# Kernel tuning notes

Hardware: AMD Instinct MI355X
Metric: run time of the kernel (lower is better)

The kernel has to match this reference:

```python
import jax, jax.numpy as jnp
import numpy as np

C = 384          # input_channels
DH = 768         # dim_hidden
WS = 7           # window size (kernel_size)
NH = 12          # num_heads
HID = 3072       # mlp hidden = dim_hidden * mlp_ratio
NP = WS * WS     # 49 patch tokens
N = NP + 1       # + 1 cls token
SCALE = (C // NH) ** -0.5
REL_DIM = 2 * WS - 1


def _rel_pos_index():
    r = np.arange(WS)
    qx, qy = np.meshgrid(r, r, indexing='ij')
    q = np.stack([qx.ravel(), qy.ravel()], -1)                 # [NP,2], row-major flatten
    rel = q[:, None, :] - q[None, :, :] + WS - 1               # [NP,NP,2], values in [0,2ws-2]
    return jnp.asarray(rel[..., 0] * REL_DIM + rel[..., 1])    # [NP,NP]

REL_IDX = _rel_pos_index()


def layer_norm(x, g, b, eps=1e-5):
    m = jnp.mean(x, axis=-1, keepdims=True)
    v = jnp.var(x, axis=-1, keepdims=True)
    return (x - m) * jax.lax.rsqrt(v + eps) * g + b


def attention(x, w_qkv, w_proj, b_proj, rel_pos=None, mask=None):
    Bx, Nx, Cx = x.shape
    qkv = (x @ w_qkv.T).reshape(Bx, Nx, 3, NH, Cx // NH).transpose(2, 0, 3, 1, 4)
    q, k, v = qkv[0], qkv[1], qkv[2]                           # [B,H,N,d]
    attn = jnp.einsum('bhqd,bhkd->bhqk', q, k) * SCALE
    if rel_pos is not None:
        bias = rel_pos[REL_IDX].transpose(2, 0, 1)[None]       # [1,NH,NP,NP]
        attn = attn.at[:, :, 1:, 1:].add(bias)                 # skip cls token row/col
    if mask is not None:
        attn = attn + mask[:, None]                            # broadcast over heads
    attn = jax.nn.softmax(attn, axis=-1)
    y = jnp.einsum('bhqk,bhkd->bhqd', attn, v).transpose(0, 2, 1, 3).reshape(Bx, Nx, Cx)
    return y @ w_proj.T + b_proj


def setup_inputs() -> dict:
    key = jax.random.key(0)
    ks = jax.random.split(key, 16)
    s = 0.02
    BNW = 2048  # B * num_windows = 32 * 64
    return {
        'out': jax.random.normal(ks[0], (BNW, N, C), jnp.float32),
        'mask': jnp.zeros((BNW, N, N), jnp.float32),
        'g0': jnp.ones((C,), jnp.float32), 'b0': jnp.zeros((C,), jnp.float32),
        'g1': jnp.ones((C,), jnp.float32), 'b1': jnp.zeros((C,), jnp.float32),
        'g2': jnp.ones((C,), jnp.float32), 'b2': jnp.zeros((C,), jnp.float32),
        'ge': jnp.ones((C,), jnp.float32), 'be': jnp.zeros((C,), jnp.float32),
        'w_qkv': jax.random.normal(ks[1], (3 * C, C), jnp.float32) * s,
        'w_proj': jax.random.normal(ks[2], (C, C), jnp.float32) * s,
        'b_proj': jnp.zeros((C,), jnp.float32),
        'rel_pos': jax.random.normal(ks[3], (REL_DIM * REL_DIM, NH), jnp.float32) * s,
        'w_fc1': jax.random.normal(ks[4], (HID, C), jnp.float32) * s,
        'b_fc1': jnp.zeros((HID,), jnp.float32),
        'w_fc2': jax.random.normal(ks[5], (DH, HID), jnp.float32) * s,
        'b_fc2': jnp.zeros((DH,), jnp.float32),
        'w_exp': jax.random.normal(ks[6], (DH, C), jnp.float32) * s,
        'b_exp': jnp.zeros((DH,), jnp.float32),
        'w_lin': jax.random.normal(ks[7], (C, DH), jnp.float32) * s,
        'b_lin': jnp.zeros((C,), jnp.float32),
        'B': 32, 'H': 56, 'W': 56,
    }


def reference(out, mask, g0, b0, g1, b1, g2, b2, ge, be,
              w_qkv, w_proj, b_proj, rel_pos,
              w_fc1, b_fc1, w_fc2, b_fc2, w_exp, b_exp, w_lin, b_lin,
              B, H, W):
    Cc = out.shape[-1]
    # cls-token attention across windows of each image
    cls = out[:, :1].reshape(B, -1, Cc)                        # [B, nw, C]
    cls = cls + attention(layer_norm(cls, g0, b0), w_qkv, w_proj, b_proj)
    cls = cls.reshape(-1, 1, Cc)
    x = jnp.concatenate([cls, out[:, 1:]], axis=1)             # [B*nw, N, C]
    # windowed patch attention with rel-pos bias + mask
    x = x + attention(layer_norm(x, g1, b1), w_qkv, w_proj, b_proj,
                      rel_pos=rel_pos, mask=mask)
    # expand path: norm -> gelu -> linear (input_channels != dim_hidden)
    identity = jax.nn.gelu(layer_norm(x, ge, be), approximate=False) @ w_exp.T + b_exp
    # mlp path: norm -> fc1 -> gelu -> fc2
    h = layer_norm(x, g2, b2)
    h = jax.nn.gelu(h @ w_fc1.T + b_fc1, approximate=False)
    h = h @ w_fc2.T + b_fc2
    tmp = identity + h                                          # [B*nw, N, DH]
    return tmp @ w_lin.T + b_lin                                # [B*nw, N, C]
```

## Files before the change

### kernel.cpp

```cpp
#include <hip/hip_runtime.h>
#include <hip/hip_bf16.h>
#include <math.h>

#define NHEADS 12
#define NTOK   50
#define NWIN   2048
#define IMGS   32
#define CDIM   384
#define QKVD   1152
#define DHID   768
#define MLPH   3072
#define KTAIL  3456
#define SCALE_F 0.17677669529663687f

typedef short short8 __attribute__((ext_vector_type(8)));
typedef short short4v __attribute__((ext_vector_type(4)));
typedef short short2v __attribute__((ext_vector_type(2)));
typedef float f32x4  __attribute__((ext_vector_type(4)));
typedef __hip_bfloat16 bf16;

__device__ __forceinline__ float rcp_fast(float x){ return __builtin_amdgcn_rcpf(x); }

__device__ __forceinline__ float gelu_f(float x){
  float z = 0.7978845608028654f*(x + 0.044715f*x*x*x);
  float e = __expf(2.0f*z);
  return 0.5f*x*(1.0f + (1.0f - 2.0f*rcp_fast(e+1.0f)));
}
__device__ __forceinline__ float gelu_fast(float x){
  float e = __expf(-1.702f*x);
  return x * rcp_fast(1.0f + e);
}
__device__ __forceinline__ short bfs(float x){
  bf16 h = __float2bfloat16(x); return *(short*)&h;
}

__global__ void cvt4_kernel(const float* s0, bf16* d0, int n0,
                            const float* s1, bf16* d1, int n1,
                            const float* s2, bf16* d2, int n2,
                            const float* s3, bf16* d3, int n3){
  int stride = gridDim.x*blockDim.x, g = blockIdx.x*blockDim.x + threadIdx.x;
  for (int i=g; i<n0; i+=stride) d0[i] = __float2bfloat16(s0[i]);
  for (int i=g; i<n1; i+=stride) d1[i] = __float2bfloat16(s1[i]);
  for (int i=g; i<n2; i+=stride) d2[i] = __float2bfloat16(s2[i]);
  for (int i=g; i<n3; i+=stride) d3[i] = __float2bfloat16(s3[i]);
}

__global__ __launch_bounds__(256) void transpose_cvt_kernel(const float* __restrict__ src,
    bf16* __restrict__ dst, int R, int Cc){
  __shared__ float tile[32][33];
  int bx = blockIdx.x, by = blockIdx.y;
  int c = threadIdx.x & 31, r0 = threadIdx.x >> 5;
  #pragma unroll
  for (int rr = r0; rr < 32; rr += 8)
    tile[rr][c] = src[(size_t)(by*32+rr)*Cc + bx*32 + c];
  __syncthreads();
  #pragma unroll
  for (int rr = r0; rr < 32; rr += 8)
    dst[(size_t)(bx*32+rr)*R + by*32 + c] = __float2bfloat16(tile[c][rr]);
}

__global__ void bias_combine_kernel(const float* __restrict__ wlin,
    const float* __restrict__ b_lin, const float* __restrict__ b_exp,
    const float* __restrict__ b_fc2, float* __restrict__ biasc){
  int i = blockIdx.x*blockDim.x + threadIdx.x;
  if (i >= CDIM) return;
  float s = b_lin[i];
  for (int d=0; d<DHID; d++) s += wlin[(size_t)i*DHID+d]*(b_exp[d]+b_fc2[d]);
  biasc[i] = s;
}

template<bool GELU>
__global__ __launch_bounds__(256) void ln_kernel(const float* __restrict__ x, long ldx,
    const float* __restrict__ g, const float* __restrict__ b,
    bf16* __restrict__ y, int rows)
{
  int row = blockIdx.x*4 + (threadIdx.x>>6);
  if (row >= rows) return;
  int l = threadIdx.x & 63;
  const float2* xr = (const float2*)(x + (size_t)row*ldx);
  float2 v[3]; float s = 0.f;
  #pragma unroll
  for (int j=0;j<3;j++){ v[j] = xr[l + 64*j]; s += v[j].x + v[j].y; }
  #pragma unroll
  for (int off=32; off; off>>=1) s += __shfl_xor(s, off, 64);
  float mean = s * (1.0f/384.0f);
  float vs = 0.f;
  #pragma unroll
  for (int j=0;j<3;j++){ float dx=v[j].x-mean, dy=v[j].y-mean; vs += dx*dx+dy*dy; }
  #pragma unroll
  for (int off=32; off; off>>=1) vs += __shfl_xor(vs, off, 64);
  float rstd = rsqrtf(vs*(1.0f/384.0f) + 1e-5f);
  short2v* yr = (short2v*)(y + (size_t)row*384);
  const float2* gv = (const float2*)g; const float2* bv = (const float2*)b;
  #pragma unroll
  for (int j=0;j<3;j++){
    float2 gg = gv[l+64*j], bb = bv[l+64*j];
    float o0 = (v[j].x-mean)*rstd*gg.x + bb.x;
    float o1 = (v[j].y-mean)*rstd*gg.y + bb.y;
    if (GELU){ o0 = gelu_f(o0); o1 = gelu_f(o1); }
    short2v pk; pk[0]=bfs(o0); pk[1]=bfs(o1);
    yr[l+64*j] = pk;
  }
}

__global__ __launch_bounds__(256) void ln_sel_kernel(const float* __restrict__ xa,
    const float* __restrict__ xbse,
    const float* __restrict__ g, const float* __restrict__ b,
    bf16* __restrict__ y, int rows)
{
  int row = blockIdx.x*4 + (threadIdx.x>>6);
  if (row >= rows) return;
  int l = threadIdx.x & 63;
  const float* src = (row % 50 == 0) ? xa : xbse;
  const float2* xr = (const float2*)(src + (size_t)row*384);
  float2 v[3]; float s = 0.f;
  #pragma unroll
  for (int j=0;j<3;j++){ v[j] = xr[l + 64*j]; s += v[j].x + v[j].y; }
  #pragma unroll
  for (int off=32; off; off>>=1) s += __shfl_xor(s, off, 64);
  float mean = s * (1.0f/384.0f);
  float vs = 0.f;
  #pragma unroll
  for (int j=0;j<3;j++){ float dx=v[j].x-mean, dy=v[j].y-mean; vs += dx*dx+dy*dy; }
  #pragma unroll
  for (int off=32; off; off>>=1) vs += __shfl_xor(vs, off, 64);
  float rstd = rsqrtf(vs*(1.0f/384.0f) + 1e-5f);
  short2v* yr = (short2v*)(y + (size_t)row*384);
  const float2* gv = (const float2*)g; const float2* bv = (const float2*)b;
  #pragma unroll
  for (int j=0;j<3;j++){
    float2 gg = gv[l+64*j], bb = bv[l+64*j];
    short2v pk;
    pk[0]=bfs((v[j].x-mean)*rstd*gg.x + bb.x);
    pk[1]=bfs((v[j].y-mean)*rstd*gg.y + bb.y);
    yr[l+64*j] = pk;
  }
}

__global__ __launch_bounds__(256) void ln_dual_kernel(const float* __restrict__ x,
    const float* __restrict__ ge, const float* __restrict__ be,
    const float* __restrict__ g2, const float* __restrict__ b2,
    bf16* __restrict__ yeo, long lde, bf16* __restrict__ y2o, int rows)
{
  int row = blockIdx.x*4 + (threadIdx.x>>6);
  if (row >= rows) return;
  int l = threadIdx.x & 63;
  const float2* xr = (const float2*)(x + (size_t)row*384);
  float2 v[3]; float s = 0.f;
  #pragma unroll
  for (int j=0;j<3;j++){ v[j] = xr[l + 64*j]; s += v[j].x + v[j].y; }
  #pragma unroll
  for (int off=32; off; off>>=1) s += __shfl_xor(s, off, 64);
  float mean = s * (1.0f/384.0f);
  float vs = 0.f;
  #pragma unroll
  for (int j=0;j<3;j++){ float dx=v[j].x-mean, dy=v[j].y-mean; vs += dx*dx+dy*dy; }
  #pragma unroll
  for (int off=32; off; off>>=1) vs += __shfl_xor(vs, off, 64);
  float rstd = rsqrtf(vs*(1.0f/384.0f) + 1e-5f);
  short2v* ye = (short2v*)(yeo + (size_t)row*lde);
  short2v* y2 = (short2v*)(y2o + (size_t)row*384);
  const float2* gev = (const float2*)ge; const float2* bev = (const float2*)be;
  const float2* g2v = (const float2*)g2; const float2* b2v = (const float2*)b2;
  #pragma unroll
  for (int j=0;j<3;j++){
    float n0 = (v[j].x-mean)*rstd, n1 = (v[j].y-mean)*rstd;
    float2 gg = gev[l+64*j], bb = bev[l+64*j];
    short2v pe; pe[0]=bfs(gelu_f(n0*gg.x+bb.x)); pe[1]=bfs(gelu_f(n1*gg.y+bb.y));
    ye[l+64*j] = pe;
    gg = g2v[l+64*j]; bb = b2v[l+64*j];
    short2v p2; p2[0]=bfs(n0*gg.x+bb.x); p2[1]=bfs(n1*gg.y+bb.y);
    y2[l+64*j] = p2;
  }
}

template<bool OUT_BF16, bool BIAS, int RES, int GELU>
__device__ __forceinline__ void gemm_dev(
    const bf16* __restrict__ A, const bf16* __restrict__ B, void* Cv,
    const float* __restrict__ bias, const void* res, const void* res2,
    int M, int N, int K, int lda, int ldb, int ldc, int ldres)
{
  __shared__ short As[3][128*32];
  __shared__ short Bs[3][128*32];
  const int t  = threadIdx.x;
  const int l  = t & 63;
  const int w  = t >> 6;
  const int wr = w >> 1, wc = w & 1;
  const int lr = l & 15, kg = l >> 4;

  const int nwg = gridDim.x * gridDim.y;
  const int lin = blockIdx.y * gridDim.x + blockIdx.x;
  const int q8 = nwg >> 3, r8 = nwg & 7;
  const int xcd = lin & 7, slot = lin >> 3;
  const int swz = (xcd < r8) ? (xcd*(q8+1) + slot) : (r8*(q8+1) + (xcd-r8)*q8 + slot);
  const int by = swz / gridDim.x, bx = swz - by*gridDim.x;

  const int bm = by * 128, bn = bx * 128;
  const short* Ag = (const short*)A;
  const short* Bg = (const short*)B;

  const int eo0 = w*1024 + l*8;
  const int rowS0 = eo0 >> 5, colS0 = eo0 & 31;
  const int eo1 = eo0 + 512;
  const int rowS1 = eo1 >> 5, colS1 = eo1 & 31;

  #define STAGE(k0, b) do { \
    __builtin_amdgcn_global_load_lds( \
      (const __attribute__((address_space(1))) void*)&Ag[(size_t)(bm+rowS0)*lda + (k0) + colS0], \
      (__attribute__((address_space(3))) void*)((char*)&As[b][0] + w*2048), 16, 0, 0); \
    __builtin_amdgcn_global_load_lds( \
      (const __attribute__((address_space(1))) void*)&Bg[(size_t)(bn+rowS0)*ldb + (k0) + colS0], \
      (__attribute__((address_space(3))) void*)((char*)&Bs[b][0] + w*2048), 16, 0, 0); \
    __builtin_amdgcn_global_load_lds( \
      (const __attribute__((address_space(1))) void*)&Ag[(size_t)(bm+rowS1)*lda + (k0) + colS1], \
      (__attribute__((address_space(3))) void*)((char*)&As[b][0] + w*2048 + 1024), 16, 0, 0); \
    __builtin_amdgcn_global_load_lds( \
      (const __attribute__((address_space(1))) void*)&Bg[(size_t)(bn+rowS1)*ldb + (k0) + colS1], \
      (__attribute__((address_space(3))) void*)((char*)&Bs[b][0] + w*2048 + 1024), 16, 0, 0); \
  } while(0)

  f32x4 acc[4][4] = {};

  STAGE(0, 0);
  STAGE(32, 1);
  asm volatile("s_waitcnt vmcnt(4)" ::: "memory");
  __builtin_amdgcn_s_barrier();

  int cur = 0, nb = 2;
  for (int k0 = 0; k0 < K; k0 += 32) {
    const bool more = (k0 + 64 < K);
    if (more) STAGE(k0 + 64, nb);

    short8 af[4], bfm[4];
    #pragma unroll
    for (int m=0;m<4;m++) af[m]  = *(const short8*)(&As[cur][(wr*64 + m*16 + lr)*32 + kg*8]);
    #pragma unroll
    for (int n=0;n<4;n++) bfm[n] = *(const short8*)(&Bs[cur][(wc*64 + n*16 + lr)*32 + kg*8]);
    __builtin_amdgcn_s_setprio(1);
    #pragma unroll
    for (int m=0;m<4;m++)
      #pragma unroll
      for (int n=0;n<4;n++)
        acc[m][n] = __builtin_amdgcn_mfma_f32_16x16x32_bf16(af[m], bfm[n], acc[m][n], 0,0,0);
    __builtin_amdgcn_s_setprio(0);

    if (more) { asm volatile("s_waitcnt vmcnt(4)" ::: "memory"); }
    else      { asm volatile("s_waitcnt vmcnt(0)" ::: "memory"); }
    __builtin_amdgcn_s_barrier();
    cur = (cur==2) ? 0 : cur+1;
    nb  = (nb==2)  ? 0 : nb+1;
  }
  #undef STAGE

  #pragma unroll
  for (int m=0;m<4;m++){
    int row0 = bm + wr*64 + m*16 + kg*4;
    #pragma unroll
    for (int n=0;n<4;n++){
      int col = bn + wc*64 + n*16 + lr;
      float bv = BIAS ? bias[col] : 0.0f;
      #pragma unroll
      for (int r=0;r<4;r++){
        float val = acc[m][n][r] + bv;
        if (RES == 1) val += ((const float*)res)[(size_t)(row0+r)*ldres + col];
        if (RES == 3){
          int grow = row0 + r;
          const float* rs = ((grow % 50) == 0) ? (const float*)res : (const float*)res2;
          val += rs[(size_t)grow*ldres + col];
        }
        if (GELU == 1) val = gelu_fast(val);
        if (OUT_BF16) ((bf16*)Cv)[(size_t)(row0+r)*ldc + col] = __float2bfloat16(val);
        else          ((float*)Cv)[(size_t)(row0+r)*ldc + col] = val;
      }
    }
  }
}

#define GEMM_K(NAME, OB, BI, RE, GE) \
__global__ __launch_bounds__(256) void NAME( \
    const bf16* __restrict__ A, const bf16* __restrict__ B, void* Cv, \
    const float* __restrict__ bias, const void* res, const void* res2, \
    int M, int N, int K, int lda, int ldc, int ldres){ \
  gemm_dev<OB,BI,RE,GE>(A,B,Cv,bias,res,res2,M,N,K,lda,K,ldc,ldres); }

GEMM_K(gemm_qkv_k,   true,  false, 0, 0)
GEMM_K(gemm_projc_k, false, true,  1, 0)
GEMM_K(gemm_projw_k, false, true,  3, 0)
GEMM_K(gemm_fc1_k,   true,  true,  0, 1)
GEMM_K(gemm_tail_k,  false, true,  0, 0)
GEMM_K(gemm_wcmb_k,  true,  false, 0, 0)

__global__ __launch_bounds__(256) void attn_cls_kernel(const bf16* __restrict__ qkv,
                                                       bf16* __restrict__ y)
{
  int img = blockIdx.x, h = blockIdx.y;
  __shared__ float q[64][33], k[64][33], v[64][33];
  __shared__ float s[64][65];
  int t = threadIdx.x;
  for (int idx=t; idx<64*32; idx+=256){
    int i = idx>>5, d = idx&31;
    const bf16* base = qkv + ((size_t)(img*64+i))*QKVD + h*32 + d;
    q[i][d] = __bfloat162float(base[0]);
    k[i][d] = __bfloat162float(base[384]);
    v[i][d] = __bfloat162float(base[768]);
  }
  __syncthreads();
  for (int idx=t; idx<64*64; idx+=256){
    int i = idx>>6, j = idx&63;
    float a = 0.f;
    #pragma unroll
    for (int d=0; d<32; d++) a += q[i][d]*k[j][d];
    s[i][j] = a * SCALE_F;
  }
  __syncthreads();
  if (t < 64){
    float m = -1e30f;
    for (int j=0;j<64;j++) m = fmaxf(m, s[t][j]);
    float sum = 0.f;
    for (int j=0;j<64;j++){ float e = __expf(s[t][j]-m); s[t][j]=e; sum+=e; }
    float inv = rcp_fast(sum);
    for (int j=0;j<64;j++) s[t][j] *= inv;
  }
  __syncthreads();
  for (int idx=t; idx<64*32; idx+=256){
    int i = idx>>5, d = idx&31;
    float a = 0.f;
    for (int j=0;j<64;j++) a += s[i][j]*v[j][d];
    y[((size_t)(img*64+i))*CDIM + h*32 + d] = __float2bfloat16(a);
  }
}

__global__ __launch_bounds__(64) void attn_win_mfma(const bf16* __restrict__ qkv,
    const float* __restrict__ mask, const float* __restrict__ rel_pos,
    bf16* __restrict__ y)
{
  const int lw = blockIdx.x, h = blockIdx.y;
  const int l = threadIdx.x;
  const int lr = l & 15, kg = l >> 4;
  __shared__ short Plds[64*72];
  __shared__ short VTl[32*72];
  __shared__ float rp[169];

  const size_t tok0 = (size_t)lw * NTOK;
  const short* qbase = (const short*)qkv;

  for (int i=l; i<169; i+=64) rp[i] = rel_pos[i*NHEADS + h];

  short8 qf[4], kf[4];
  #pragma unroll
  for (int n=0;n<4;n++){
    int qt = 16*n + lr;
    if (qt < 50) qf[n] = *(const short8*)&qbase[(tok0+qt)*QKVD + h*32 + kg*8];
    else         qf[n] = short8(0);
  }
  #pragma unroll
  for (int m=0;m<4;m++){
    int kt = 16*m + lr;
    if (kt < 50) kf[m] = *(const short8*)&qbase[(tok0+kt)*QKVD + 384 + h*32 + kg*8];
    else         kf[m] = short8(0);
  }

  {
    short vv[32];
    if (l < 50){
      const short8* vp = (const short8*)&qbase[(tok0+l)*QKVD + 768 + h*32];
      #pragma unroll
      for (int jj=0;jj<4;jj++){ short8 xv = vp[jj];
        #pragma unroll
        for (int e=0;e<8;e++) vv[jj*8+e] = xv[e]; }
    } else {
      #pragma unroll
      for (int d=0; d<32; d++) vv[d]=0;
    }
    #pragma unroll
    for (int d=0; d<32; d++) VTl[d*72 + l] = vv[d];
  }

  f32x4 sacc[4][4] = {};
  #pragma unroll
  for (int m=0;m<4;m++)
    #pragma unroll
    for (int n=0;n<4;n++)
      sacc[m][n] = __builtin_amdgcn_mfma_f32_16x16x32_bf16(kf[m], qf[n], sacc[m][n], 0,0,0);

  const float* mrow = mask + (size_t)lw*2500;
  float sv[4][4][4];
  #pragma unroll
  for (int m=0;m<4;m++){
    #pragma unroll
    for (int r=0;r<4;r++){
      int kt = 16*m + 4*kg + r;
      #pragma unroll
      for (int n=0;n<4;n++){
        int qt = 16*n + lr;
        float a;
        if (kt < 50 && qt < 50){
          a = sacc[m][n][r] * SCALE_F;
          if (kt>=1 && qt>=1){
            int qi=qt-1, kj=kt-1;
            int ridx = ((qi/7)-(kj/7)+6)*13 + (qi%7)-(kj%7)+6;
            a += rp[ridx];
          }
          a += mrow[qt*50+kt];
        } else a = -1e30f;
        sv[m][r][n] = a;
      }
    }
  }

  #pragma unroll
  for (int n=0;n<4;n++){
    float mx = -1e30f;
    #pragma unroll
    for (int m=0;m<4;m++)
      #pragma unroll
      for (int r=0;r<4;r++) mx = fmaxf(mx, sv[m][r][n]);
    mx = fmaxf(mx, __shfl_xor(mx, 16));
    mx = fmaxf(mx, __shfl_xor(mx, 32));
    float sum = 0.f;
    float pv[4][4];
    #pragma unroll
    for (int m=0;m<4;m++)
      #pragma unroll
      for (int r=0;r<4;r++){ float p = __expf(sv[m][r][n]-mx); pv[m][r]=p; sum+=p; }
    sum += __shfl_xor(sum, 16);
    sum += __shfl_xor(sum, 32);
    float inv = rcp_fast(sum);
    int qrow = (16*n + lr)*72;
    #pragma unroll
    for (int m=0;m<4;m++){
      short4v pk;
      #pragma unroll
      for (int r=0;r<4;r++) pk[r] = bfs(pv[m][r]*inv);
      *(short4v*)&Plds[qrow + 16*m + 4*kg] = pk;
    }
  }
  __syncthreads();

  f32x4 oacc[2][4] = {};
  #pragma unroll
  for (int ks=0; ks<2; ks++){
    short8 pf[4];
    #pragma unroll
    for (int n=0;n<4;n++)
      pf[n] = *(const short8*)&Plds[(16*n+lr)*72 + 32*ks + kg*8];
    #pragma unroll
    for (int md=0; md<2; md++){
      short8 vf = *(const short8*)&VTl[(16*md+lr)*72 + 32*ks + kg*8];
      #pragma unroll
      for (int n=0;n<4;n++)
        oacc[md][n] = __builtin_amdgcn_mfma_f32_16x16x32_bf16(vf, pf[n], oacc[md][n], 0,0,0);
    }
  }

  short* yb = (short*)y;
  #pragma unroll
  for (int n=0;n<4;n++){
    int qt = 16*n + lr;
    if (qt >= 50) continue;
    #pragma unroll
    for (int md=0; md<2; md++){
      short4v pk;
      #pragma unroll
      for (int r=0;r<4;r++) pk[r] = bfs(oacc[md][n][r]);
      *(short4v*)&yb[(tok0+qt)*CDIM + h*32 + 16*md + 4*kg] = pk;
    }
  }
}

extern "C" void kernel_launch(void* const* d_in, const int* in_sizes, int n_in,
                              void* d_out, int out_size, void* d_ws, size_t ws_size,
                              hipStream_t stream)
{
  const float* x_in   = (const float*)d_in[0];
  const float* maskp  = (const float*)d_in[1];
  const float* g0 = (const float*)d_in[2];  const float* b0 = (const float*)d_in[3];
  const float* g1 = (const float*)d_in[4];  const float* b1 = (const float*)d_in[5];
  const float* g2 = (const float*)d_in[6];  const float* b2 = (const float*)d_in[7];
  const float* ge = (const float*)d_in[8];  const float* be = (const float*)d_in[9];
  const float* w_qkv = (const float*)d_in[10];
  const float* w_proj= (const float*)d_in[11];
  const float* b_proj= (const float*)d_in[12];
  const float* rel_pos=(const float*)d_in[13];
  const float* w_fc1 = (const float*)d_in[14];
  const float* b_fc1 = (const float*)d_in[15];
  const float* w_fc2 = (const float*)d_in[16];
  const float* b_fc2 = (const float*)d_in[17];
  const float* w_exp = (const float*)d_in[18];
  const float* b_exp = (const float*)d_in[19];
  const float* w_lin = (const float*)d_in[20];
  const float* b_lin = (const float*)d_in[21];
  float* dout = (float*)d_out;

  const size_t NT = (size_t)NWIN * NTOK;

  size_t off = 0;
  auto alloc = [&](size_t bytes)->void* {
    void* p = (char*)d_ws + off;
    off += (bytes + 255) & ~(size_t)255;
    return p;
  };

  bf16* wqkv_b = (bf16*)alloc((size_t)QKVD*CDIM*2);
  bf16* wproj_b= (bf16*)alloc((size_t)CDIM*CDIM*2);
  bf16* wfc1_b = (bf16*)alloc((size_t)MLPH*CDIM*2);
  bf16* wlin_b = (bf16*)alloc((size_t)CDIM*DHID*2);
  bf16* wexpT_b= (bf16*)alloc((size_t)CDIM*DHID*2);
  bf16* wfc2T_b= (bf16*)alloc((size_t)MLPH*DHID*2);
  bf16* W_comb = (bf16*)alloc((size_t)CDIM*KTAIL*2);
  float* biasc = (float*)alloc((size_t)CDIM*4);
  float* xb    = (float*)alloc(NT*CDIM*4);
  bf16* clsln  = (bf16*)alloc((size_t)NWIN*CDIM*2);
  bf16* qkvcls = (bf16*)alloc((size_t)NWIN*QKVD*2);
  bf16* ycls   = (bf16*)alloc((size_t)NWIN*CDIM*2);

  int CH_W = 2048;
  const size_t per_window = 422400ull;
  while (CH_W > 128 && off + (size_t)CH_W*per_window + 16384 > ws_size) CH_W >>= 1;
  const int CH_T = CH_W * NTOK;

  bf16*  xln   = (bf16*) alloc((size_t)CH_T*CDIM*2);
  bf16*  ybfc  = (bf16*) alloc((size_t)CH_T*CDIM*2);
  bf16*  h1ext = (bf16*) alloc((size_t)CH_T*KTAIL*2);
  bf16*  qkvc  = h1ext;

  cvt4_kernel<<<512, 256, 0, stream>>>(
      w_qkv, wqkv_b, QKVD*CDIM,  w_proj, wproj_b, CDIM*CDIM,
      w_fc1, wfc1_b, MLPH*CDIM,  w_lin,  wlin_b,  CDIM*DHID);
  transpose_cvt_kernel<<<dim3(CDIM/32, DHID/32), 256, 0, stream>>>(w_exp, wexpT_b, DHID, CDIM);
  transpose_cvt_kernel<<<dim3(MLPH/32, DHID/32), 256, 0, stream>>>(w_fc2, wfc2T_b, DHID, MLPH);
  bias_combine_kernel<<<6, 64, 0, stream>>>(w_lin, b_lin, b_exp, b_fc2, biasc);
  gemm_wcmb_k<<<dim3(CDIM/128, CDIM/128), 256, 0, stream>>>(
      wlin_b, wexpT_b, W_comb, nullptr, nullptr, nullptr, CDIM, CDIM, DHID, DHID, KTAIL, 0);
  gemm_wcmb_k<<<dim3(MLPH/128, CDIM/128), 256, 0, stream>>>(
      wlin_b, wfc2T_b, W_comb + 384, nullptr, nullptr, nullptr, CDIM, MLPH, DHID, DHID, KTAIL, 0);

  ln_kernel<false><<<NWIN/4, 256, 0, stream>>>(x_in, (long)NTOK*CDIM, g0, b0, clsln, NWIN);
  gemm_qkv_k<<<dim3(QKVD/128, NWIN/128), 256, 0, stream>>>(
      clsln, wqkv_b, qkvcls, nullptr, nullptr, nullptr, NWIN, QKVD, CDIM, CDIM, QKVD, 0);
  attn_cls_kernel<<<dim3(IMGS, NHEADS), 256, 0, stream>>>(qkvcls, ycls);
  gemm_projc_k<<<dim3(CDIM/128, NWIN/128), 256, 0, stream>>>(
      ycls, wproj_b, xb, b_proj, x_in, nullptr, NWIN, CDIM, CDIM, CDIM, NTOK*CDIM, NTOK*CDIM);

  const int nch = NWIN / CH_W;
  for (int c = 0; c < nch; c++){
    int w0 = c * CH_W;
    size_t t0 = (size_t)w0 * NTOK;
    float* xbc = xb + t0*CDIM;
    const float* xinc = x_in + t0*CDIM;
    float* doutc = dout + t0*CDIM;
    int MT = CH_T, MB = CH_T/128;

    ln_sel_kernel<<<MT/4, 256, 0, stream>>>(xbc, xinc, g1, b1, xln, MT);
    gemm_qkv_k<<<dim3(QKVD/128, MB), 256, 0, stream>>>(
        xln, wqkv_b, qkvc, nullptr, nullptr, nullptr, MT, QKVD, CDIM, CDIM, QKVD, 0);
    attn_win_mfma<<<dim3(CH_W, NHEADS), 64, 0, stream>>>(
        qkvc, maskp + (size_t)w0*2500, rel_pos, ybfc);
    gemm_projw_k<<<dim3(CDIM/128, MB), 256, 0, stream>>>(
        ybfc, wproj_b, xbc, b_proj, xbc, xinc, MT, CDIM, CDIM, CDIM, CDIM, CDIM);

    ln_dual_kernel<<<MT/4, 256, 0, stream>>>(xbc, ge, be, g2, b2, h1ext, KTAIL, ybfc, MT);

    gemm_fc1_k<<<dim3(MLPH/128, MB), 256, 0, stream>>>(
        ybfc, wfc1_b, h1ext + 384, b_fc1, nullptr, nullptr, MT, MLPH, CDIM, CDIM, KTAIL, 0);

    gemm_tail_k<<<dim3(CDIM/128, MB), 256, 0, stream>>>(
        h1ext, W_comb, doutc, biasc, nullptr, nullptr, MT, CDIM, KTAIL, KTAIL, CDIM, 0);
  }
}
```

Baseline: 1.654 ms.

## Process all heads per window block and stage mask in shared memory

The windowed attention kernel now launches one 128-thread block per window instead of one 64-thread block per (window, head). The block loads the 50x50 mask into LDS once, and each of its two wavefronts loops over six heads, so the mask is reused across all twelve heads instead of being re-read from global memory per head. The tail GEMM is also specialised with a compile-time ldb constant. In exchange the grid has twelve times fewer blocks, each with more LDS and serial work, which may reduce parallelism and latency hiding.

```diff
diff --git a/kernel.cpp b/kernel.cpp
--- a/kernel.cpp
+++ b/kernel.cpp
@@ -287,8 +287,14 @@
 GEMM_K(gemm_projc_k, false, true,  1, 0)
 GEMM_K(gemm_projw_k, false, true,  3, 0)
 GEMM_K(gemm_fc1_k,   true,  true,  0, 1)
-GEMM_K(gemm_tail_k,  false, true,  0, 0)
 GEMM_K(gemm_wcmb_k,  true,  false, 0, 0)
+
+__global__ __launch_bounds__(256) void gemm_tail_k(
+    const bf16* __restrict__ A, const bf16* __restrict__ B, void* Cv,
+    const float* __restrict__ bias, const void* res, const void* res2,
+    int M, int N, int K, int lda, int ldc, int ldres){
+  gemm_dev<false,true,0,0>(A,B,Cv,bias,res,res2,M,N,K,lda,KTAIL,ldc,ldres);
+}
 
 __global__ __launch_bounds__(256) void attn_cls_kernel(const bf16* __restrict__ qkv,
                                                        bf16* __restrict__ y)
@@ -330,140 +336,153 @@
   }
 }
 
-__global__ __launch_bounds__(64) void attn_win_mfma(const bf16* __restrict__ qkv,
+__global__ __launch_bounds__(128) void attn_win_mfma(const bf16* __restrict__ qkv,
     const float* __restrict__ mask, const float* __restrict__ rel_pos,
     bf16* __restrict__ y)
 {
-  const int lw = blockIdx.x, h = blockIdx.y;
-  const int l = threadIdx.x;
+  const int lw = blockIdx.x;
+  const int tid = threadIdx.x;
+  const int w = tid >> 6;
+  const int l = tid & 63;
   const int lr = l & 15, kg = l >> 4;
-  __shared__ short Plds[64*72];
-  __shared__ short VTl[32*72];
-  __shared__ float rp[169];
+
+  __shared__ float msk[2500];
+  __shared__ float rp_w[2][169];
+  __shared__ short PldsA[2][64*72];
+  __shared__ short VTlA[2][32*72];
 
   const size_t tok0 = (size_t)lw * NTOK;
   const short* qbase = (const short*)qkv;
 
-  for (int i=l; i<169; i+=64) rp[i] = rel_pos[i*NHEADS + h];
-
-  short8 qf[4], kf[4];
-  #pragma unroll
-  for (int n=0;n<4;n++){
-    int qt = 16*n + lr;
-    if (qt < 50) qf[n] = *(const short8*)&qbase[(tok0+qt)*QKVD + h*32 + kg*8];
-    else         qf[n] = short8(0);
-  }
-  #pragma unroll
-  for (int m=0;m<4;m++){
-    int kt = 16*m + lr;
-    if (kt < 50) kf[m] = *(const short8*)&qbase[(tok0+kt)*QKVD + 384 + h*32 + kg*8];
-    else         kf[m] = short8(0);
-  }
-
-  {
-    short vv[32];
-    if (l < 50){
-      const short8* vp = (const short8*)&qbase[(tok0+l)*QKVD + 768 + h*32];
-      #pragma unroll
-      for (int jj=0;jj<4;jj++){ short8 xv = vp[jj];
-        #pragma unroll
-        for (int e=0;e<8;e++) vv[jj*8+e] = xv[e]; }
-    } else {
-      #pragma unroll
-      for (int d=0; d<32; d++) vv[d]=0;
-    }
-    #pragma unroll
-    for (int d=0; d<32; d++) VTl[d*72 + l] = vv[d];
-  }
-
-  f32x4 sacc[4][4] = {};
-  #pragma unroll
-  for (int m=0;m<4;m++)
-    #pragma unroll
-    for (int n=0;n<4;n++)
-      sacc[m][n] = __builtin_amdgcn_mfma_f32_16x16x32_bf16(kf[m], qf[n], sacc[m][n], 0,0,0);
-
-  const float* mrow = mask + (size_t)lw*2500;
-  float sv[4][4][4];
-  #pragma unroll
-  for (int m=0;m<4;m++){
-    #pragma unroll
-    for (int r=0;r<4;r++){
-      int kt = 16*m + 4*kg + r;
-      #pragma unroll
-      for (int n=0;n<4;n++){
-        int qt = 16*n + lr;
-        float a;
-        if (kt < 50 && qt < 50){
-          a = sacc[m][n][r] * SCALE_F;
-          if (kt>=1 && qt>=1){
-            int qi=qt-1, kj=kt-1;
-            int ridx = ((qi/7)-(kj/7)+6)*13 + (qi%7)-(kj%7)+6;
-            a += rp[ridx];
-          }
-          a += mrow[qt*50+kt];
-        } else a = -1e30f;
-        sv[m][r][n] = a;
+  for (int i = tid; i < 2500; i += 128) msk[i] = mask[(size_t)lw*2500 + i];
+  __syncthreads();
+
+  short* Plds = &PldsA[w][0];
+  short* VTl  = &VTlA[w][0];
+  float* rp   = &rp_w[w][0];
+
+  for (int hh = 0; hh < 6; hh++){
+    const int h = w*6 + hh;
+
+    for (int i = l; i < 169; i += 64) rp[i] = rel_pos[i*NHEADS + h];
+
+    short8 qf[4], kf[4];
+    #pragma unroll
+    for (int n=0;n<4;n++){
+      int qt = 16*n + lr;
+      if (qt < 50) qf[n] = *(const short8*)&qbase[(tok0+qt)*QKVD + h*32 + kg*8];
+      else         qf[n] = short8(0);
+    }
+    #pragma unroll
+    for (int m=0;m<4;m++){
+      int kt = 16*m + lr;
+      if (kt < 50) kf[m] = *(const short8*)&qbase[(tok0+kt)*QKVD + 384 + h*32 + kg*8];
+      else         kf[m] = short8(0);
+    }
+
+    {
+      short vv[32];
+      if (l < 50){
+        const short8* vp = (const short8*)&qbase[(tok0+l)*QKVD + 768 + h*32];
+        #pragma unroll
+        for (int jj=0;jj<4;jj++){ short8 xv = vp[jj];
+          #pragma unroll
+          for (int e=0;e<8;e++) vv[jj*8+e] = xv[e]; }
+      } else {
+        #pragma unroll
+        for (int d=0; d<32; d++) vv[d]=0;
       }
-    }
-  }
-
-  #pragma unroll
-  for (int n=0;n<4;n++){
-    float mx = -1e30f;
+      #pragma unroll
+      for (int d=0; d<32; d++) VTl[d*72 + l] = vv[d];
+    }
+
+    f32x4 sacc[4][4] = {};
     #pragma unroll
     for (int m=0;m<4;m++)
       #pragma unroll
-      for (int r=0;r<4;r++) mx = fmaxf(mx, sv[m][r][n]);
-    mx = fmaxf(mx, __shfl_xor(mx, 16));
-    mx = fmaxf(mx, __shfl_xor(mx, 32));
-    float sum = 0.f;
-    float pv[4][4];
-    #pragma unroll
-    for (int m=0;m<4;m++)
-      #pragma unroll
-      for (int r=0;r<4;r++){ float p = __expf(sv[m][r][n]-mx); pv[m][r]=p; sum+=p; }
-    sum += __shfl_xor(sum, 16);
-    sum += __shfl_xor(sum, 32);
-    float inv = rcp_fast(sum);
-    int qrow = (16*n + lr)*72;
+      for (int n=0;n<4;n++)
+        sacc[m][n] = __builtin_amdgcn_mfma_f32_16x16x32_bf16(kf[m], qf[n], sacc[m][n], 0,0,0);
+
+    float sv[4][4][4];
     #pragma unroll
     for (int m=0;m<4;m++){
-      short4v pk;
-      #pragma unroll
-      for (int r=0;r<4;r++) pk[r] = bfs(pv[m][r]*inv);
-      *(short4v*)&Plds[qrow + 16*m + 4*kg] = pk;
-    }
-  }
-  __syncthreads();
-
-  f32x4 oacc[2][4] = {};
-  #pragma unroll
-  for (int ks=0; ks<2; ks++){
-    short8 pf[4];
-    #pragma unroll
-    for (int n=0;n<4;n++)
-      pf[n] = *(const short8*)&Plds[(16*n+lr)*72 + 32*ks + kg*8];
-    #pragma unroll
-    for (int md=0; md<2; md++){
-      short8 vf = *(const short8*)&VTl[(16*md+lr)*72 + 32*ks + kg*8];
+      #pragma unroll
+      for (int r=0;r<4;r++){
+        int kt = 16*m + 4*kg + r;
+        #pragma unroll
+        for (int n=0;n<4;n++){
+          int qt = 16*n + lr;
+          float a;
+          if (kt < 50 && qt < 50){
+            a = sacc[m][n][r] * SCALE_F;
+            if (kt>=1 && qt>=1){
+              int qi=qt-1, kj=kt-1;
+              int ridx = ((qi/7)-(kj/7)+6)*13 + (qi%7)-(kj%7)+6;
+              a += rp[ridx];
+            }
+            a += msk[qt*50+kt];
+          } else a = -1e30f;
+          sv[m][r][n] = a;
+        }
+      }
+    }
+
+    #pragma unroll
+    for (int n=0;n<4;n++){
+      float mx = -1e30f;
+      #pragma unroll
+      for (int m=0;m<4;m++)
+        #pragma unroll
+        for (int r=0;r<4;r++) mx = fmaxf(mx, sv[m][r][n]);
+      mx = fmaxf(mx, __shfl_xor(mx, 16));
+      mx = fmaxf(mx, __shfl_xor(mx, 32));
+      float sum = 0.f;
+      float pv[4][4];
+      #pragma unroll
+      for (int m=0;m<4;m++)
+        #pragma unroll
+        for (int r=0;r<4;r++){ float p = __expf(sv[m][r][n]-mx); pv[m][r]=p; sum+=p; }
+      sum += __shfl_xor(sum, 16);
+      sum += __shfl_xor(sum, 32);
+      float inv = rcp_fast(sum);
+      int qrow = (16*n + lr)*72;
+      #pragma unroll
+      for (int m=0;m<4;m++){
+        short4v pk;
+        #pragma unroll
+        for (int r=0;r<4;r++) pk[r] = bfs(pv[m][r]*inv);
+        *(short4v*)&Plds[qrow + 16*m + 4*kg] = pk;
+      }
+    }
+
+    f32x4 oacc[2][4] = {};
+    #pragma unroll
+    for (int ks=0; ks<2; ks++){
+      short8 pf[4];
       #pragma unroll
       for (int n=0;n<4;n++)
-        oacc[md][n] = __builtin_amdgcn_mfma_f32_16x16x32_bf16(vf, pf[n], oacc[md][n], 0,0,0);
-    }
-  }
-
-  short* yb = (short*)y;
-  #pragma unroll
-  for (int n=0;n<4;n++){
-    int qt = 16*n + lr;
-    if (qt >= 50) continue;
-    #pragma unroll
-    for (int md=0; md<2; md++){
-      short4v pk;
-      #pragma unroll
-      for (int r=0;r<4;r++) pk[r] = bfs(oacc[md][n][r]);
-      *(short4v*)&yb[(tok0+qt)*CDIM + h*32 + 16*md + 4*kg] = pk;
+        pf[n] = *(const short8*)&Plds[(16*n+lr)*72 + 32*ks + kg*8];
+      #pragma unroll
+      for (int md=0; md<2; md++){
+        short8 vf = *(const short8*)&VTl[(16*md+lr)*72 + 32*ks + kg*8];
+        #pragma unroll
+        for (int n=0;n<4;n++)
+          oacc[md][n] = __builtin_amdgcn_mfma_f32_16x16x32_bf16(vf, pf[n], oacc[md][n], 0,0,0);
+      }
+    }
+
+    short* yb = (short*)y;
+    #pragma unroll
+    for (int n=0;n<4;n++){
+      int qt = 16*n + lr;
+      if (qt >= 50) continue;
+      #pragma unroll
+      for (int md=0; md<2; md++){
+        short4v pk;
+        #pragma unroll
+        for (int r=0;r<4;r++) pk[r] = bfs(oacc[md][n][r]);
+        *(short4v*)&yb[(tok0+qt)*CDIM + h*32 + 16*md + 4*kg] = pk;
+      }
     }
   }
 }
@@ -554,7 +573,7 @@
     ln_sel_kernel<<<MT/4, 256, 0, stream>>>(xbc, xinc, g1, b1, xln, MT);
     gemm_qkv_k<<<dim3(QKVD/128, MB), 256, 0, stream>>>(
         xln, wqkv_b, qkvc, nullptr, nullptr, nullptr, MT, QKVD, CDIM, CDIM, QKVD, 0);
-    attn_win_mfma<<<dim3(CH_W, NHEADS), 64, 0, stream>>>(
+    attn_win_mfma<<<dim3(CH_W), 128, 0, stream>>>(
         qkvc, maskp + (size_t)w0*2500, rel_pos, ybfc);
     gemm_projw_k<<<dim3(CDIM/128, MB), 256, 0, stream>>>(
         ybfc, wproj_b, xbc, b_proj, xbc, xinc, MT, CDIM, CDIM, CDIM, CDIM, CDIM);
```

New measurement: 1.603 ms. 1.03x faster.
